# Kernel tuning notes

Hardware: AMD Instinct MI355X
Metric: run time of the kernel (lower is better)

Reference implementation:

```python
import jax, jax.numpy as jnp
from jax import lax
import numpy as np

BN_INV = 1.0 / np.sqrt(1.0 + 1e-5)  # eval-mode BatchNorm with running mean 0, var 1


def gather_points(x, idx):
    # x: [B, N, C]; idx: [B, ...] int -> [B, ..., C]
    bi = jnp.arange(x.shape[0]).reshape((x.shape[0],) + (1,) * (idx.ndim - 1))
    return x[bi, idx]


def fps(xyz, npoint):
    # furthest point sampling starting at index 0. xyz: [B, N, 3] -> [B, npoint] int32
    B, N, _ = xyz.shape

    def step(carry, _):
        dist, last = carry
        lx = jnp.take_along_axis(xyz, last[:, None, None], axis=1)  # [B,1,3]
        d = jnp.sum((xyz - lx) ** 2, axis=-1)                       # [B,N]
        dist = jnp.minimum(dist, d)
        nxt = jnp.argmax(dist, axis=-1).astype(jnp.int32)
        return (dist, nxt), nxt

    first = jnp.zeros((B,), jnp.int32)
    dist0 = jnp.full((B, N), 1e10, xyz.dtype)
    _, rest = lax.scan(step, (dist0, first), None, length=npoint - 1)
    return jnp.concatenate([first[None], rest], axis=0).T  # [B, npoint]


def ball_query(radius, nsample, xyz, new_xyz):
    # first nsample points (in index order) within radius of each query; pad with first hit
    N = xyz.shape[1]
    d2 = jnp.sum((new_xyz[:, :, None, :] - xyz[:, None, :, :]) ** 2, axis=-1)  # [B,S,N]
    mask = d2 < radius * radius
    key = jnp.where(mask, jnp.arange(N, dtype=jnp.int32), N)
    idx_sorted = jnp.sort(key, axis=-1)[..., :nsample]                          # [B,S,ns]
    cnt = jnp.sum(mask, axis=-1, keepdims=True)                                 # [B,S,1]
    idx = jnp.where(jnp.arange(nsample) < cnt, idx_sorted, idx_sorted[..., :1])
    return jnp.minimum(idx, N - 1)


def bn_relu(x, gamma, beta):
    # eval-mode BN (running mean 0 / var 1) + ReLU; channels on the last axis
    return jax.nn.relu(x * (gamma * BN_INV) + beta)


def sa_module(xyz, feats, npoint, radius, nsample, layers):
    # xyz [B,N,3], feats [B,C,N] -> (new_xyz [B,S,3], new_feats [B,Cout,S])
    fidx = fps(xyz, npoint)
    new_xyz = gather_points(xyz, fidx)                      # [B,S,3]
    gidx = ball_query(radius, nsample, xyz, new_xyz)        # [B,S,ns]
    g_xyz = gather_points(xyz, gidx) - new_xyz[:, :, None, :]   # [B,S,ns,3]
    g_feat = gather_points(jnp.swapaxes(feats, 1, 2), gidx)     # [B,S,ns,C]
    h = jnp.concatenate([g_xyz, g_feat], axis=-1)               # use_xyz=True
    for (w, g, b) in layers:                                    # shared MLP (1x1 conv2d+BN+ReLU)
        h = bn_relu(jnp.einsum('bsnc,oc->bsno', h, w), g, b)
    return new_xyz, jnp.swapaxes(jnp.max(h, axis=2), 1, 2)      # max-pool over nsample


def fp_module(unk_xyz, kn_xyz, unk_feats, kn_feats, layers):
    # three-NN weighted interpolation (squared distances, as the CUDA op) + unit conv MLP
    d2 = jnp.sum((unk_xyz[:, :, None, :] - kn_xyz[:, None, :, :]) ** 2, axis=-1)
    neg, idx = lax.top_k(-d2, 3)                 # 3 nearest known points
    w = 1.0 / (-neg + 1e-8)
    w = w / jnp.sum(w, axis=-1, keepdims=True)   # [B,Nu,3]
    kf = gather_points(jnp.swapaxes(kn_feats, 1, 2), idx)       # [B,Nu,3,C]
    interp = jnp.sum(kf * w[..., None], axis=2)                 # [B,Nu,C]
    h = jnp.concatenate([interp, jnp.swapaxes(unk_feats, 1, 2)], axis=-1)
    for (wt, g, b) in layers:
        h = bn_relu(jnp.einsum('bnc,oc->bno', h, wt), g, b)
    return jnp.swapaxes(h, 1, 2)                                # [B,Cout,Nu]


def setup_inputs() -> dict:
    key = jax.random.key(0)
    it = iter(jax.random.split(key, 80))
    B, N = 16, 4096
    d = {
        'xyz': jax.random.uniform(next(it), (B, N, 3), jnp.float32) * 0.3,
        'feats': jax.random.normal(next(it), (B, N, 3), jnp.float32),
    }
    specs = {'sa1': [(6, 64), (64, 128)], 'sa2': [(131, 128), (128, 256)],
             'sa3': [(259, 256), (256, 512)], 'fp3': [(768, 256), (256, 256)],
             'fp2': [(384, 128), (128, 128)], 'fp1': [(131, 128), (128, 128)]}
    for name, layers in specs.items():
        for i, (ci, co) in enumerate(layers):
            d[f'{name}_w{i}'] = jax.random.normal(next(it), (co, ci), jnp.float32) / np.sqrt(ci)
            d[f'{name}_g{i}'] = 1.0 + 0.1 * jax.random.normal(next(it), (co,), jnp.float32)
            d[f'{name}_b{i}'] = 0.1 * jax.random.normal(next(it), (co,), jnp.float32)
    d['fin_w'] = jax.random.normal(next(it), (512, 128), jnp.float32) / np.sqrt(128.0)
    d['fin_b'] = 0.1 * jax.random.normal(next(it), (512,), jnp.float32)
    d['fin_g'] = 1.0 + 0.1 * jax.random.normal(next(it), (512,), jnp.float32)
    d['fin_be'] = 0.1 * jax.random.normal(next(it), (512,), jnp.float32)
    return d


def reference(xyz, feats,
              sa1_w0, sa1_g0, sa1_b0, sa1_w1, sa1_g1, sa1_b1,
              sa2_w0, sa2_g0, sa2_b0, sa2_w1, sa2_g1, sa2_b1,
              sa3_w0, sa3_g0, sa3_b0, sa3_w1, sa3_g1, sa3_b1,
              fp3_w0, fp3_g0, fp3_b0, fp3_w1, fp3_g1, fp3_b1,
              fp2_w0, fp2_g0, fp2_b0, fp2_w1, fp2_g1, fp2_b1,
              fp1_w0, fp1_g0, fp1_b0, fp1_w1, fp1_g1, fp1_b1,
              fin_w, fin_b, fin_g, fin_be):
    f0 = jnp.swapaxes(feats, 1, 2)  # [B,3,N], channel-first like the torch module
    l1x, l1f = sa_module(xyz, f0, 256, 0.04, 16,
                         [(sa1_w0, sa1_g0, sa1_b0), (sa1_w1, sa1_g1, sa1_b1)])
    l2x, l2f = sa_module(l1x, l1f, 64, 0.08, 16,
                         [(sa2_w0, sa2_g0, sa2_b0), (sa2_w1, sa2_g1, sa2_b1)])
    l3x, l3f = sa_module(l2x, l2f, 16, 0.16, 16,
                         [(sa3_w0, sa3_g0, sa3_b0), (sa3_w1, sa3_g1, sa3_b1)])
    l2f = fp_module(l2x, l3x, l2f, l3f, [(fp3_w0, fp3_g0, fp3_b0), (fp3_w1, fp3_g1, fp3_b1)])
    l1f = fp_module(l1x, l2x, l1f, l2f, [(fp2_w0, fp2_g0, fp2_b0), (fp2_w1, fp2_g1, fp2_b1)])
    l0f = fp_module(xyz, l1x, f0, l1f, [(fp1_w0, fp1_g0, fp1_b0), (fp1_w1, fp1_g1, fp1_b1)])
    # final Conv1d(128->512, bias) + BN + ReLU
    h = jnp.einsum('bcn,oc->bon', l0f, fin_w) + fin_b[None, :, None]
    h = jax.nn.relu(h * (fin_g * BN_INV)[None, :, None] + fin_be[None, :, None])
    B, C, N = h.shape
    return jnp.swapaxes(h, 1, 2).reshape(B * N, C)  # un-batched per-point features
```

## Files before the change

### kernel.cpp

```cpp
#include <hip/hip_runtime.h>

#define DEVI __device__ __forceinline__
typedef unsigned long long u64;

static constexpr float BN_INV_F = 0.9999950000374997f;

DEVI float d2rn(float ax, float ay, float az, float bx, float by, float bz) {
    float dx = __fsub_rn(ax, bx), dy = __fsub_rn(ay, by), dz = __fsub_rn(az, bz);
    return __fadd_rn(__fadd_rn(__fmul_rn(dx, dx), __fmul_rn(dy, dy)), __fmul_rn(dz, dz));
}

DEVI u64 shfl_xor_u64(u64 x, int m) {
    unsigned lo = (unsigned)x, hi = (unsigned)(x >> 32);
    lo = (unsigned)__shfl_xor((int)lo, m, 64);
    hi = (unsigned)__shfl_xor((int)hi, m, 64);
    return ((u64)hi << 32) | lo;
}
DEVI u64 umin64(u64 a, u64 b) { return a < b ? a : b; }
DEVI u64 umax64(u64 a, u64 b) { return a > b ? a : b; }

template <int N, int NPOINT, int BS>
DEVI void fps_impl(const float* __restrict__ xyz, int* __restrict__ fidx) {
    constexpr int PPT = N / BS;
    constexpr int NW = BS / 64;
    __shared__ float4 xs4[N];
    __shared__ u64 wmax[2][NW > 1 ? NW : 1];
    const int t = threadIdx.x, b = blockIdx.x, lane = t & 63, wv = t >> 6;
    const float* xb = xyz + (size_t)b * N * 3;
    for (int p = t; p < N; p += BS)
        xs4[p] = make_float4(xb[p * 3], xb[p * 3 + 1], xb[p * 3 + 2], 0.f);
    if (t == 0) fidx[b * NPOINT] = 0;
    __syncthreads();
    float px[PPT], py[PPT], pz[PPT], dist[PPT];
#pragma unroll
    for (int i = 0; i < PPT; ++i) {
        float4 v = xs4[i * BS + t];
        px[i] = v.x; py[i] = v.y; pz[i] = v.z;
        dist[i] = 1e10f;
    }
    float4 q0 = xs4[0];
    float qx = q0.x, qy = q0.y, qz = q0.z;
    for (int it = 1; it < NPOINT; ++it) {
        float bestd = -1.f;
        unsigned bestidx = 0u;
#pragma unroll
        for (int i = 0; i < PPT; ++i) {
            float d = d2rn(px[i], py[i], pz[i], qx, qy, qz);
            float nd = fminf(dist[i], d);
            dist[i] = nd;
            if (nd > bestd) { bestd = nd; bestidx = (unsigned)(i * BS + t); }
        }
        u64 best = ((u64)__float_as_uint(bestd) << 32) | (0xFFFFFFFFu - bestidx);
#pragma unroll
        for (int m = 1; m < 64; m <<= 1) best = umax64(best, shfl_xor_u64(best, m));
        if constexpr (NW > 1) {
            if (lane == 0) wmax[it & 1][wv] = best;
            __syncthreads();
            u64 m2 = wmax[it & 1][lane & (NW - 1)];
#pragma unroll
            for (int m = 1; m < NW; m <<= 1) m2 = umax64(m2, shfl_xor_u64(m2, m));
            best = m2;
        }
        int p = (int)(0xFFFFFFFFu - (unsigned)best);
        float4 qv = xs4[p];
        qx = qv.x; qy = qv.y; qz = qv.z;
        if (t == 0) fidx[b * NPOINT + it] = p;
    }
}

__global__ __launch_bounds__(256) void fps1_kernel(const float* __restrict__ x, int* __restrict__ f) { fps_impl<4096, 256, 256>(x, f); }
__global__ __launch_bounds__(64)  void fps2_kernel(const float* __restrict__ x, int* __restrict__ f) { fps_impl<256, 64, 64>(x, f); }
__global__ __launch_bounds__(64)  void fps3_kernel(const float* __restrict__ x, int* __restrict__ f) { fps_impl<64, 16, 64>(x, f); }

template <int TR, int XSTR, int KMAIN, int CIM, int CIF, int MOFF, int CO, int MODE,
          bool SIDE, int SOFF, int OSTR>
DEVI void gemm_phase(float* __restrict__ Xs, float* __restrict__ Ws,
                     const float* __restrict__ W,
                     const float* __restrict__ sA, const float* __restrict__ sB,
                     const float* __restrict__ fbias,
                     float* __restrict__ gout, int r0,
                     unsigned* __restrict__ mp, const float* __restrict__ side, int t) {
    constexpr int RT = TR / 16;
    constexpr int NCOL = (CO / 16 < 8) ? (CO / 16) : 8;
    constexpr int ROWS = 16 * NCOL;
    constexpr int CC = CO / ROWS;
    constexpr int NCH = KMAIN / 8;
    constexpr int NQ = CC * NCH;
    constexpr int PRE = ROWS / 32;
    constexpr int XSTR4 = XSTR / 4;
    constexpr int AC = (MODE == 0) ? CC : 1;
    const int tx = t & 15, ty = t >> 4;
    const int swz = ty & 3;
    float acc[AC][RT][NCOL];
    if constexpr (MODE == 0) {
#pragma unroll
        for (int a = 0; a < AC; ++a)
#pragma unroll
            for (int r = 0; r < RT; ++r)
#pragma unroll
                for (int i = 0; i < NCOL; ++i) acc[a][r][i] = 0.f;
    }
    float pre[PRE];
#pragma unroll
    for (int i = 0; i < PRE; ++i) {
        int e = t + 256 * i, row = e >> 3, kk = e & 7;
        pre[i] = (kk < CIM) ? W[(size_t)row * CIF + MOFF + kk] : 0.f;
    }
#pragma unroll
    for (int i = 0; i < PRE; ++i) {
        int e = t + 256 * i;
        Ws[(e >> 3) * 12 + (e & 7)] = pre[i];
    }
#pragma unroll
    for (int cc = 0; cc < CC; ++cc) {
        if constexpr (MODE != 0) {
#pragma unroll
            for (int r = 0; r < RT; ++r)
#pragma unroll
                for (int i = 0; i < NCOL; ++i) acc[0][r][i] = 0.f;
        }
        for (int kc = 0; kc < NCH; ++kc) {
            const int qq = cc * NCH + kc, buf = kc & 1;
            __syncthreads();
            if (qq + 1 < NQ) {
                const int cn = (qq + 1) / NCH, kn = ((qq + 1) % NCH) * 8;
#pragma unroll
                for (int i = 0; i < PRE; ++i) {
                    int e = t + 256 * i, row = e >> 3, k = kn + (e & 7);
                    pre[i] = (k < CIM) ? W[(size_t)(cn * ROWS + row) * CIF + MOFF + k] : 0.f;
                }
            }
            const float* wsb = Ws + buf * (ROWS * 12);
#pragma unroll
            for (int k4i = 0; k4i < 2; ++k4i) {
                const int c4 = kc * 2 + k4i;
                float4 wv[NCOL];
#pragma unroll
                for (int i = 0; i < NCOL; ++i)
                    wv[i] = *(const float4*)&wsb[(tx + 16 * i) * 12 + k4i * 4];
                float4 xv[RT];
#pragma unroll
                for (int r = 0; r < RT; ++r)
                    xv[r] = *(const float4*)&Xs[((ty * RT + r) * XSTR4 + (c4 ^ swz)) * 4];
#pragma unroll
                for (int r = 0; r < RT; ++r)
#pragma unroll
                    for (int i = 0; i < NCOL; ++i) {
                        const int a = (MODE == 0) ? cc : 0;
                        acc[a][r][i] = fmaf(xv[r].x, wv[i].x, acc[a][r][i]);
                        acc[a][r][i] = fmaf(xv[r].y, wv[i].y, acc[a][r][i]);
                        acc[a][r][i] = fmaf(xv[r].z, wv[i].z, acc[a][r][i]);
                        acc[a][r][i] = fmaf(xv[r].w, wv[i].w, acc[a][r][i]);
                    }
            }
            if (qq + 1 < NQ) {
                float* wsn = Ws + (buf ^ 1) * (ROWS * 12);
#pragma unroll
                for (int i = 0; i < PRE; ++i) {
                    int e = t + 256 * i;
                    wsn[(e >> 3) * 12 + (e & 7)] = pre[i];
                }
            }
        }
        if constexpr (MODE == 1) {
#pragma unroll
            for (int i = 0; i < NCOL; ++i) {
                int c = cc * ROWS + tx + 16 * i;
                float bia = fbias ? fbias[c] : 0.f;
                float sc = sA[c] * BN_INV_F, be = sB[c];
#pragma unroll
                for (int r = 0; r < RT; ++r) {
                    float val = fmaxf(fmaf(acc[0][r][i] + bia, sc, be), 0.f);
                    gout[(size_t)(r0 + ty * RT + r) * OSTR + c] = val;
                }
            }
        } else if constexpr (MODE == 2) {
#pragma unroll
            for (int i = 0; i < NCOL; ++i) {
                int c = cc * ROWS + tx + 16 * i;
                float sc = sA[c] * BN_INV_F, bb = sB[c];
#pragma unroll
                for (int r = 0; r < RT; ++r) {
                    float val = fmaxf(fmaf(acc[0][r][i], sc, bb), 0.f);
                    atomicMax(&mp[((ty * RT + r) >> 4) * CO + c], __float_as_uint(val));
                }
            }
        }
    }
    if constexpr (MODE == 0) {
        if constexpr (SIDE) {
#pragma unroll
            for (int cc = 0; cc < AC; ++cc)
#pragma unroll
                for (int i = 0; i < NCOL; ++i) {
                    int c = cc * ROWS + tx + 16 * i;
#pragma unroll
                    for (int j = 0; j < 3; ++j) {
                        float wj = W[(size_t)c * CIF + SOFF + j];
#pragma unroll
                        for (int r = 0; r < RT; ++r)
                            acc[cc][r][i] = fmaf(side[(ty * RT + r) * 3 + j], wj,
                                                 acc[cc][r][i]);
                    }
                }
        }
        __syncthreads();
#pragma unroll
        for (int cc = 0; cc < AC; ++cc)
#pragma unroll
            for (int i = 0; i < NCOL; ++i) {
                int c = cc * ROWS + tx + 16 * i;
                float sc = sA[c] * BN_INV_F, bb = sB[c];
#pragma unroll
                for (int r = 0; r < RT; ++r) {
                    int row = ty * RT + r;
                    Xs[(row * XSTR4 + ((c >> 2) ^ swz)) * 4 + (c & 3)] =
                        fmaxf(fmaf(acc[cc][r][i], sc, bb), 0.f);
                }
            }
        __syncthreads();
    }
}

template <int N, int S, int CIN, int C1, int C2, int TR, bool USE_SIDE>
DEVI void sa_impl(const float* __restrict__ xyz, const float* __restrict__ feats,
                  const int* __restrict__ fidx,
                  const float* __restrict__ w0, const float* __restrict__ g0, const float* __restrict__ b0,
                  const float* __restrict__ w1, const float* __restrict__ g1, const float* __restrict__ b1,
                  float* __restrict__ oxyz, float* __restrict__ ofeat, float r2) {
    constexpr int QPB = TR / 16;
    constexpr int CIF = 3 + CIN;
    constexpr int KMAIN = USE_SIDE ? CIN : 16;
    constexpr int XSTR = (KMAIN > C1) ? KMAIN : C1;
    constexpr int XSTR4 = XSTR / 4;
    constexpr int RT = TR / 16;
    __shared__ __align__(16) float Xs[TR * XSTR];
    __shared__ __align__(16) float Ws[2 * 128 * 12];
    __shared__ int ids[QPB][16];
    __shared__ float qp[QPB][3];
    __shared__ unsigned mp[QPB * C2];
    __shared__ float side[USE_SIDE ? TR * 3 : 4];
    const int t = threadIdx.x, lane = t & 63, wv = t >> 6;
    const int q0 = blockIdx.x * QPB;
    for (int q = wv; q < QPB; q += 4) {
        const int sq = q0 + q, bb = sq / S;
        const float* xb = xyz + (size_t)bb * N * 3;
        const int qi = fidx[sq];
        const float qx = xb[qi * 3], qy = xb[qi * 3 + 1], qz = xb[qi * 3 + 2];
        if (lane == 0) {
            qp[q][0] = qx; qp[q][1] = qy; qp[q][2] = qz;
            float* op = oxyz + (size_t)sq * 3;
            op[0] = qx; op[1] = qy; op[2] = qz;
        }
        int base = 0;
        for (int seg = 0; seg < N; seg += 64) {
            const int p = seg + lane;
            float d = d2rn(xb[p * 3], xb[p * 3 + 1], xb[p * 3 + 2], qx, qy, qz);
            bool hit = d < r2;
            u64 mask = __ballot(hit);
            int before = (int)__popcll(mask & ((1ull << lane) - 1ull));
            if (hit && base + before < 16) ids[q][base + before] = p;
            base += (int)__popcll(mask);
            if (base >= 16) break;
        }
        if (lane == 0) {
            int cnt = base < 16 ? base : 16;
            int first = ids[q][0];
            for (int r = cnt; r < 16; ++r) ids[q][r] = first;
        }
    }
    __syncthreads();
    if constexpr (!USE_SIDE) {
        for (int e = t; e < TR * 16; e += 256) {
            int j = e >> 4, c = e & 15;
            int q = j >> 4, p = ids[q][j & 15];
            int bb = (q0 + q) / S;
            float v = 0.f;
            if (c < 3) v = __fsub_rn(xyz[((size_t)bb * N + p) * 3 + c], qp[q][c]);
            else if (c < 6) v = feats[((size_t)bb * N + p) * CIN + (c - 3)];
            Xs[(j * XSTR4 + ((c >> 2) ^ ((j / RT) & 3))) * 4 + (c & 3)] = v;
        }
    } else {
        constexpr int C4N = CIN / 4;
        for (int e = t; e < TR * C4N; e += 256) {
            int j = e / C4N, c4 = e % C4N;
            int q = j >> 4, p = ids[q][j & 15];
            int bb = (q0 + q) / S;
            float4 v = *(const float4*)&feats[((size_t)bb * N + p) * CIN + c4 * 4];
            *(float4*)&Xs[(j * XSTR4 + (c4 ^ ((j / RT) & 3))) * 4] = v;
        }
        for (int e = t; e < TR * 3; e += 256) {
            int j = e / 3, c = e % 3;
            int q = j >> 4, p = ids[q][j & 15];
            int bb = (q0 + q) / S;
            side[e] = __fsub_rn(xyz[((size_t)bb * N + p) * 3 + c], qp[q][c]);
        }
    }
    for (int e = t; e < QPB * C2; e += 256) mp[e] = 0u;
    gemm_phase<TR, XSTR, KMAIN, (USE_SIDE ? CIN : 6), CIF, (USE_SIDE ? 3 : 0),
               C1, 0, USE_SIDE, 0, 0>(Xs, Ws, w0, g0, b0, nullptr, nullptr, 0,
                                      nullptr, side, t);
    gemm_phase<TR, XSTR, C1, C1, C1, 0, C2, 2, false, 0, 0>(
        Xs, Ws, w1, g1, b1, nullptr, nullptr, 0, mp, nullptr, t);
    __syncthreads();
    for (int e = t; e < QPB * C2; e += 256)
        ofeat[(size_t)q0 * C2 + e] = __uint_as_float(mp[e]);
}

#define SA_ARGS const float* __restrict__ xyz, const float* __restrict__ feats, \
                const int* __restrict__ fidx, \
                const float* __restrict__ w0, const float* __restrict__ g0, const float* __restrict__ b0, \
                const float* __restrict__ w1, const float* __restrict__ g1, const float* __restrict__ b1, \
                float* __restrict__ oxyz, float* __restrict__ ofeat, float r2
__global__ __launch_bounds__(256) void sa1_kernel(SA_ARGS) {
    sa_impl<4096, 256, 3, 64, 128, 64, false>(xyz, feats, fidx, w0, g0, b0, w1, g1, b1, oxyz, ofeat, r2);
}
__global__ __launch_bounds__(256) void sa2_kernel(SA_ARGS) {
    sa_impl<256, 64, 128, 128, 256, 64, true>(xyz, feats, fidx, w0, g0, b0, w1, g1, b1, oxyz, ofeat, r2);
}
__global__ __launch_bounds__(256) void sa3_kernel(SA_ARGS) {
    sa_impl<64, 16, 256, 256, 512, 16, true>(xyz, feats, fidx, w0, g0, b0, w1, g1, b1, oxyz, ofeat, r2);
}

template <int M, int CK, int CU, int C1, int C2, int TR>
DEVI void fp_impl(const float* __restrict__ uxyz, const float* __restrict__ kxyz,
                  const float* __restrict__ ufeat, const float* __restrict__ kfeat,
                  const float* __restrict__ w0, const float* __restrict__ g0, const float* __restrict__ b0,
                  const float* __restrict__ w1, const float* __restrict__ g1, const float* __restrict__ b1,
                  float* __restrict__ out, int NU) {
    constexpr int CH = CK + CU;
    constexpr int XSTR = CH;
    constexpr int XSTR4 = XSTR / 4;
    constexpr int RT = TR / 16;
    __shared__ __align__(16) float Xs[TR * XSTR];
    __shared__ __align__(16) float Ws[2 * 128 * 12];
    __shared__ float kxs[M * 3];
    const int t = threadIdx.x, lane = t & 63, wv = t >> 6;
    const int r0 = blockIdx.x * TR;
    const int b = r0 / NU;
    for (int e = t; e < M * 3; e += 256) kxs[e] = kxyz[(size_t)b * M * 3 + e];
    __syncthreads();
    for (int j = wv; j < TR; j += 4) {
        const int r = r0 + j;
        const int sw = (j / RT) & 3;
        const float* up = uxyz + (size_t)r * 3;
        float ux = up[0], uy = up[1], uz = up[2];
        u64 a0 = ~0ull, a1 = ~0ull, a2 = ~0ull;
        for (int k = lane; k < M; k += 64) {
            float d = d2rn(kxs[k * 3], kxs[k * 3 + 1], kxs[k * 3 + 2], ux, uy, uz);
            u64 key = ((u64)__float_as_uint(d) << 32) | (unsigned)k;
            if (key < a0)      { a2 = a1; a1 = a0; a0 = key; }
            else if (key < a1) { a2 = a1; a1 = key; }
            else if (key < a2) { a2 = key; }
        }
#pragma unroll
        for (int m = 1; m < 64; m <<= 1) {
            u64 b0k = shfl_xor_u64(a0, m), b1k = shfl_xor_u64(a1, m), b2k = shfl_xor_u64(a2, m);
            u64 c0 = umin64(a0, b0k);
            u64 c1 = umin64(umax64(a0, b0k), umin64(a1, b1k));
            u64 c2 = umin64(umin64(umax64(a1, b0k), umax64(a0, b1k)), umin64(a2, b2k));
            a0 = c0; a1 = c1; a2 = c2;
        }
        int s0 = (int)(unsigned)a0, s1 = (int)(unsigned)a1, s2 = (int)(unsigned)a2;
        float d0 = __uint_as_float((unsigned)(a0 >> 32));
        float d1 = __uint_as_float((unsigned)(a1 >> 32));
        float dd2 = __uint_as_float((unsigned)(a2 >> 32));
        float wa = 1.0f / (d0 + 1e-8f), wb = 1.0f / (d1 + 1e-8f), wc = 1.0f / (dd2 + 1e-8f);
        float sum = (wa + wb) + wc;
        wa /= sum; wb /= sum; wc /= sum;
        const float* kb = kfeat + (size_t)b * M * CK;
        for (int c4 = lane; c4 < CK / 4; c4 += 64) {
            float4 va = *(const float4*)(kb + (size_t)s0 * CK + c4 * 4);
            float4 vb = *(const float4*)(kb + (size_t)s1 * CK + c4 * 4);
            float4 vc = *(const float4*)(kb + (size_t)s2 * CK + c4 * 4);
            float4 rr;
            rr.x = va.x * wa + vb.x * wb + vc.x * wc;
            rr.y = va.y * wa + vb.y * wb + vc.y * wc;
            rr.z = va.z * wa + vb.z * wb + vc.z * wc;
            rr.w = va.w * wa + vb.w * wb + vc.w * wc;
            *(float4*)&Xs[(j * XSTR4 + (c4 ^ sw)) * 4] = rr;
        }
        for (int c4 = CK / 4 + lane; c4 < CH / 4; c4 += 64) {
            float4 v = *(const float4*)&ufeat[(size_t)r * CU + (c4 * 4 - CK)];
            *(float4*)&Xs[(j * XSTR4 + (c4 ^ sw)) * 4] = v;
        }
    }
    gemm_phase<TR, XSTR, CH, CH, CH, 0, C1, 0, false, 0, 0>(
        Xs, Ws, w0, g0, b0, nullptr, nullptr, 0, nullptr, nullptr, t);
    gemm_phase<TR, XSTR, C1, C1, C1, 0, C2, 1, false, 0, C2>(
        Xs, Ws, w1, g1, b1, nullptr, out, r0, nullptr, nullptr, t);
}

#define FP_ARGS const float* __restrict__ uxyz, const float* __restrict__ kxyz, \
                const float* __restrict__ ufeat, const float* __restrict__ kfeat, \
                const float* __restrict__ w0, const float* __restrict__ g0, const float* __restrict__ b0, \
                const float* __restrict__ w1, const float* __restrict__ g1, const float* __restrict__ b1, \
                float* __restrict__ out, int NU
__global__ __launch_bounds__(256) void fp3_kernel(FP_ARGS) {
    fp_impl<16, 512, 256, 256, 256, 16>(uxyz, kxyz, ufeat, kfeat, w0, g0, b0, w1, g1, b1, out, NU);
}
__global__ __launch_bounds__(256) void fp2_kernel(FP_ARGS) {
    fp_impl<64, 256, 128, 128, 128, 16>(uxyz, kxyz, ufeat, kfeat, w0, g0, b0, w1, g1, b1, out, NU);
}

__global__ __launch_bounds__(256) void fp1_mlp_kernel(
    const float* __restrict__ uxyz, const float* __restrict__ kxyz,
    const float* __restrict__ ufeat3, const float* __restrict__ kfeat,
    const float* __restrict__ w0, const float* __restrict__ g0, const float* __restrict__ b0,
    const float* __restrict__ w1, const float* __restrict__ g1, const float* __restrict__ b1,
    float* __restrict__ out) {
    constexpr int TR = 128, M = 256, CK = 128;
    __shared__ __align__(16) float Xs[TR * 128];
    __shared__ __align__(16) float Ws[2 * 128 * 12];
    __shared__ float side[TR * 3];
    __shared__ float wgt2[TR * 2];
    __shared__ unsigned pidx[TR];
    const int t = threadIdx.x;
    const int r0 = blockIdx.x * TR;
    const int b = r0 >> 12;
    for (int e = t; e < TR * 3; e += 256) side[e] = ufeat3[(size_t)r0 * 3 + e];
    const int g = t >> 2, sub = t & 3;
    const float* kb3 = kxyz + (size_t)b * M * 3;
    for (int row = g; row < TR; row += 64) {
        const float* up = uxyz + (size_t)(r0 + row) * 3;
        float ux = up[0], uy = up[1], uz = up[2];
        u64 a0 = ~0ull, a1 = ~0ull, a2 = ~0ull;
        for (int k = sub; k < M; k += 4) {
            float d = d2rn(kb3[k * 3], kb3[k * 3 + 1], kb3[k * 3 + 2], ux, uy, uz);
            u64 key = ((u64)__float_as_uint(d) << 32) | (unsigned)k;
            if (key < a0)      { a2 = a1; a1 = a0; a0 = key; }
            else if (key < a1) { a2 = a1; a1 = key; }
            else if (key < a2) { a2 = key; }
        }
#pragma unroll
        for (int m = 1; m < 4; m <<= 1) {
            u64 b0k = shfl_xor_u64(a0, m), b1k = shfl_xor_u64(a1, m), b2k = shfl_xor_u64(a2, m);
            u64 c0 = umin64(a0, b0k);
            u64 c1 = umin64(umax64(a0, b0k), umin64(a1, b1k));
            u64 c2 = umin64(umin64(umax64(a1, b0k), umax64(a0, b1k)), umin64(a2, b2k));
            a0 = c0; a1 = c1; a2 = c2;
        }
        if (sub == 0) {
            unsigned s0 = (unsigned)a0 & 255u, s1 = (unsigned)a1 & 255u, s2 = (unsigned)a2 & 255u;
            float d0 = __uint_as_float((unsigned)(a0 >> 32));
            float d1 = __uint_as_float((unsigned)(a1 >> 32));
            float dd2 = __uint_as_float((unsigned)(a2 >> 32));
            float wa = 1.0f / (d0 + 1e-8f), wb = 1.0f / (d1 + 1e-8f), wc = 1.0f / (dd2 + 1e-8f);
            float sum = (wa + wb) + wc;
            wa /= sum; wb /= sum;
            pidx[row] = s0 | (s1 << 8) | (s2 << 16);
            wgt2[row * 2] = wa; wgt2[row * 2 + 1] = wb;
        }
    }
    __syncthreads();
    const float* kfb = kfeat + (size_t)b * M * CK;
    for (int e = t; e < TR * 32; e += 256) {
        int j = e >> 5, c4 = e & 31;
        unsigned u = pidx[j];
        int s0 = u & 255, s1 = (u >> 8) & 255, s2 = (u >> 16) & 255;
        float wa = wgt2[j * 2], wb = wgt2[j * 2 + 1], wc = 1.0f - wa - wb;
        float4 va = *(const float4*)(kfb + (size_t)s0 * CK + c4 * 4);
        float4 vb = *(const float4*)(kfb + (size_t)s1 * CK + c4 * 4);
        float4 vc = *(const float4*)(kfb + (size_t)s2 * CK + c4 * 4);
        float4 rr;
        rr.x = va.x * wa + vb.x * wb + vc.x * wc;
        rr.y = va.y * wa + vb.y * wb + vc.y * wc;
        rr.z = va.z * wa + vb.z * wb + vc.z * wc;
        rr.w = va.w * wa + vb.w * wb + vc.w * wc;
        *(float4*)&Xs[(j * 32 + (c4 ^ ((j >> 3) & 3))) * 4] = rr;
    }
    gemm_phase<TR, 128, 128, 128, 131, 0, 128, 0, true, 128, 0>(
        Xs, Ws, w0, g0, b0, nullptr, nullptr, 0, nullptr, side, t);
    gemm_phase<TR, 128, 128, 128, 128, 0, 128, 1, false, 0, 512>(
        Xs, Ws, w1, g1, b1, nullptr, out, r0, nullptr, nullptr, t);
}

__global__ __launch_bounds__(256) void fin_kernel(
    float* io,
    const float* __restrict__ fw, const float* __restrict__ fb,
    const float* __restrict__ fg, const float* __restrict__ fbe) {
    __shared__ __align__(16) float Xs[128 * 128];
    __shared__ __align__(16) float Ws[2 * 128 * 12];
    const int t = threadIdx.x, tx = t & 15, ty = t >> 4;
    const int r0 = blockIdx.x * 128;
    const int swz = ty & 3;
    for (int e = t; e < 128 * 32; e += 256) {
        int j = e >> 5, c4 = e & 31;
        float4 v = *(const float4*)&io[(size_t)(r0 + j) * 512 + c4 * 4];
        *(float4*)&Xs[(j * 32 + (c4 ^ ((j >> 3) & 3))) * 4] = v;
    }
    for (int nt = 0; nt < 4; ++nt) {
        const int c0 = nt * 128;
        float acc[8][8];
#pragma unroll
        for (int r = 0; r < 8; ++r)
#pragma unroll
            for (int i = 0; i < 8; ++i) acc[r][i] = 0.f;
        float wpre[4];
#pragma unroll
        for (int i = 0; i < 4; ++i) {
            int e = t + 256 * i, row = e >> 3, kk = e & 7;
            wpre[i] = fw[(size_t)(c0 + row) * 128 + kk];
        }
#pragma unroll
        for (int i = 0; i < 4; ++i) {
            int e = t + 256 * i;
            Ws[(e >> 3) * 12 + (e & 7)] = wpre[i];
        }
        for (int kc = 0; kc < 16; ++kc) {
            const int buf = kc & 1;
            __syncthreads();
            if (kc < 15) {
                const int kn = (kc + 1) * 8;
#pragma unroll
                for (int i = 0; i < 4; ++i) {
                    int e = t + 256 * i, row = e >> 3, kk = e & 7;
                    wpre[i] = fw[(size_t)(c0 + row) * 128 + kn + kk];
                }
            }
            const float* wsb = Ws + buf * 1536;
#pragma unroll
            for (int k4i = 0; k4i < 2; ++k4i) {
                const int c4 = kc * 2 + k4i;
                float4 wv[8];
#pragma unroll
                for (int i = 0; i < 8; ++i)
                    wv[i] = *(const float4*)&wsb[(tx + 16 * i) * 12 + k4i * 4];
                float4 xv[8];
#pragma unroll
                for (int r = 0; r < 8; ++r)
                    xv[r] = *(const float4*)&Xs[((ty * 8 + r) * 32 + (c4 ^ swz)) * 4];
#pragma unroll
                for (int r = 0; r < 8; ++r)
#pragma unroll
                    for (int i = 0; i < 8; ++i) {
                        acc[r][i] = fmaf(xv[r].x, wv[i].x, acc[r][i]);
                        acc[r][i] = fmaf(xv[r].y, wv[i].y, acc[r][i]);
                        acc[r][i] = fmaf(xv[r].z, wv[i].z, acc[r][i]);
                        acc[r][i] = fmaf(xv[r].w, wv[i].w, acc[r][i]);
                    }
            }
            if (kc < 15) {
                float* wsn = Ws + (buf ^ 1) * 1536;
#pragma unroll
                for (int i = 0; i < 4; ++i) {
                    int e = t + 256 * i;
                    wsn[(e >> 3) * 12 + (e & 7)] = wpre[i];
                }
            }
        }
#pragma unroll
        for (int i = 0; i < 8; ++i) {
            int c = c0 + tx + 16 * i;
            float bia = fb[c], sc = fg[c] * BN_INV_F, be = fbe[c];
#pragma unroll
            for (int r = 0; r < 8; ++r) {
                float val = fmaxf(fmaf(acc[r][i] + bia, sc, be), 0.f);
                io[(size_t)(r0 + ty * 8 + r) * 512 + c] = val;
            }
        }
    }
}

extern "C" void kernel_launch(void* const* d_in, const int* in_sizes, int n_in,
                              void* d_out, int out_size, void* d_ws, size_t ws_size,
                              hipStream_t stream) {
    (void)in_sizes; (void)n_in; (void)out_size; (void)ws_size;
    const float* xyz   = (const float*)d_in[0];
    const float* feats = (const float*)d_in[1];
    const float* sa1_w0 = (const float*)d_in[2];
    const float* sa1_g0 = (const float*)d_in[3];
    const float* sa1_b0 = (const float*)d_in[4];
    const float* sa1_w1 = (const float*)d_in[5];
    const float* sa1_g1 = (const float*)d_in[6];
    const float* sa1_b1 = (const float*)d_in[7];
    const float* sa2_w0 = (const float*)d_in[8];
    const float* sa2_g0 = (const float*)d_in[9];
    const float* sa2_b0 = (const float*)d_in[10];
    const float* sa2_w1 = (const float*)d_in[11];
    const float* sa2_g1 = (const float*)d_in[12];
    const float* sa2_b1 = (const float*)d_in[13];
    const float* sa3_w0 = (const float*)d_in[14];
    const float* sa3_g0 = (const float*)d_in[15];
    const float* sa3_b0 = (const float*)d_in[16];
    const float* sa3_w1 = (const float*)d_in[17];
    const float* sa3_g1 = (const float*)d_in[18];
    const float* sa3_b1 = (const float*)d_in[19];
    const float* fp3_w0 = (const float*)d_in[20];
    const float* fp3_g0 = (const float*)d_in[21];
    const float* fp3_b0 = (const float*)d_in[22];
    const float* fp3_w1 = (const float*)d_in[23];
    const float* fp3_g1 = (const float*)d_in[24];
    const float* fp3_b1 = (const float*)d_in[25];
    const float* fp2_w0 = (const float*)d_in[26];
    const float* fp2_g0 = (const float*)d_in[27];
    const float* fp2_b0 = (const float*)d_in[28];
    const float* fp2_w1 = (const float*)d_in[29];
    const float* fp2_g1 = (const float*)d_in[30];
    const float* fp2_b1 = (const float*)d_in[31];
    const float* fp1_w0 = (const float*)d_in[32];
    const float* fp1_g0 = (const float*)d_in[33];
    const float* fp1_b0 = (const float*)d_in[34];
    const float* fp1_w1 = (const float*)d_in[35];
    const float* fp1_g1 = (const float*)d_in[36];
    const float* fp1_b1 = (const float*)d_in[37];
    const float* fin_w  = (const float*)d_in[38];
    const float* fin_b  = (const float*)d_in[39];
    const float* fin_g  = (const float*)d_in[40];
    const float* fin_be = (const float*)d_in[41];

    float* ws = (float*)d_ws;
    float* l1x  = ws;
    float* l1f  = l1x + 12288;
    float* l2x  = l1f + 524288;
    float* l2f  = l2x + 3072;
    float* l3x  = l2f + 262144;
    float* l3f  = l3x + 768;
    float* l2fb = l3f + 131072;
    float* l1fb = l2fb + 262144;
    int* fidx1 = (int*)(l1fb + 524288);
    int* fidx2 = fidx1 + 4096;
    int* fidx3 = fidx2 + 1024;

    const float R2_1 = (float)(0.04 * 0.04);
    const float R2_2 = (float)(0.08 * 0.08);
    const float R2_3 = (float)(0.16 * 0.16);

    fps1_kernel<<<16, 256, 0, stream>>>(xyz, fidx1);
    sa1_kernel<<<1024, 256, 0, stream>>>(
        xyz, feats, fidx1, sa1_w0, sa1_g0, sa1_b0, sa1_w1, sa1_g1, sa1_b1,
        l1x, l1f, R2_1);

    fps2_kernel<<<16, 64, 0, stream>>>(l1x, fidx2);
    sa2_kernel<<<256, 256, 0, stream>>>(
        l1x, l1f, fidx2, sa2_w0, sa2_g0, sa2_b0, sa2_w1, sa2_g1, sa2_b1,
        l2x, l2f, R2_2);

    fps3_kernel<<<16, 64, 0, stream>>>(l2x, fidx3);
    sa3_kernel<<<256, 256, 0, stream>>>(
        l2x, l2f, fidx3, sa3_w0, sa3_g0, sa3_b0, sa3_w1, sa3_g1, sa3_b1,
        l3x, l3f, R2_3);

    fp3_kernel<<<64, 256, 0, stream>>>(
        l2x, l3x, l2f, l3f, fp3_w0, fp3_g0, fp3_b0, fp3_w1, fp3_g1, fp3_b1,
        l2fb, 64);

    fp2_kernel<<<256, 256, 0, stream>>>(
        l1x, l2x, l1f, l2fb, fp2_w0, fp2_g0, fp2_b0, fp2_w1, fp2_g1, fp2_b1,
        l1fb, 256);

    fp1_mlp_kernel<<<512, 256, 0, stream>>>(
        xyz, l1x, feats, l1fb, fp1_w0, fp1_g0, fp1_b0, fp1_w1, fp1_g1, fp1_b1,
        (float*)d_out);

    fin_kernel<<<512, 256, 0, stream>>>(
        (float*)d_out, fin_w, fin_b, fin_g, fin_be);
}
```

Measured before the change: 805.0 us.

## Fuse all three FPS stages into one kernel keeping sampled points in LDS

Replaces the three separate furthest-point-sampling kernels with one kernel per batch. After the level-1 FPS it runs the level-2 and level-3 FPS on a single wavefront, using the selected points held in shared memory, and writes l1x/l2x/l3x directly. The SA kernels no longer write the sampled coordinates. This removes two kernel launches and their serialized dependency on the SA kernels, at the cost of three wavefronts idling while the small FPS stages run.

```diff
diff --git a/kernel.cpp b/kernel.cpp
--- a/kernel.cpp
+++ b/kernel.cpp
@@ -19,17 +19,20 @@
 DEVI u64 umin64(u64 a, u64 b) { return a < b ? a : b; }
 DEVI u64 umax64(u64 a, u64 b) { return a > b ? a : b; }
 
-template <int N, int NPOINT, int BS>
-DEVI void fps_impl(const float* __restrict__ xyz, int* __restrict__ fidx) {
-    constexpr int PPT = N / BS;
-    constexpr int NW = BS / 64;
+__global__ __launch_bounds__(256) void fps_all_kernel(
+    const float* __restrict__ xyz, int* __restrict__ fidx1,
+    int* __restrict__ fidx2, int* __restrict__ fidx3,
+    float* __restrict__ l1x, float* __restrict__ l2x, float* __restrict__ l3x) {
+    constexpr int N = 4096, NP1 = 256, BS = 256, PPT = 16, NW = 4;
     __shared__ float4 xs4[N];
-    __shared__ u64 wmax[2][NW > 1 ? NW : 1];
+    __shared__ float4 sel1[NP1];
+    __shared__ float4 sel2[64];
+    __shared__ u64 wmax[2][NW];
     const int t = threadIdx.x, b = blockIdx.x, lane = t & 63, wv = t >> 6;
     const float* xb = xyz + (size_t)b * N * 3;
     for (int p = t; p < N; p += BS)
         xs4[p] = make_float4(xb[p * 3], xb[p * 3 + 1], xb[p * 3 + 2], 0.f);
-    if (t == 0) fidx[b * NPOINT] = 0;
+    if (t == 0) fidx1[b * NP1] = 0;
     __syncthreads();
     float px[PPT], py[PPT], pz[PPT], dist[PPT];
 #pragma unroll
@@ -40,7 +43,12 @@
     }
     float4 q0 = xs4[0];
     float qx = q0.x, qy = q0.y, qz = q0.z;
-    for (int it = 1; it < NPOINT; ++it) {
+    if (t == 0) {
+        sel1[0] = q0;
+        float* o = l1x + (size_t)b * NP1 * 3;
+        o[0] = q0.x; o[1] = q0.y; o[2] = q0.z;
+    }
+    for (int it = 1; it < NP1; ++it) {
         float bestd = -1.f;
         unsigned bestidx = 0u;
 #pragma unroll
@@ -53,24 +61,91 @@
         u64 best = ((u64)__float_as_uint(bestd) << 32) | (0xFFFFFFFFu - bestidx);
 #pragma unroll
         for (int m = 1; m < 64; m <<= 1) best = umax64(best, shfl_xor_u64(best, m));
-        if constexpr (NW > 1) {
-            if (lane == 0) wmax[it & 1][wv] = best;
-            __syncthreads();
-            u64 m2 = wmax[it & 1][lane & (NW - 1)];
-#pragma unroll
-            for (int m = 1; m < NW; m <<= 1) m2 = umax64(m2, shfl_xor_u64(m2, m));
-            best = m2;
-        }
+        if (lane == 0) wmax[it & 1][wv] = best;
+        __syncthreads();
+        u64 m2 = wmax[it & 1][lane & (NW - 1)];
+#pragma unroll
+        for (int m = 1; m < NW; m <<= 1) m2 = umax64(m2, shfl_xor_u64(m2, m));
+        best = m2;
         int p = (int)(0xFFFFFFFFu - (unsigned)best);
         float4 qv = xs4[p];
         qx = qv.x; qy = qv.y; qz = qv.z;
-        if (t == 0) fidx[b * NPOINT + it] = p;
-    }
-}
-
-__global__ __launch_bounds__(256) void fps1_kernel(const float* __restrict__ x, int* __restrict__ f) { fps_impl<4096, 256, 256>(x, f); }
-__global__ __launch_bounds__(64)  void fps2_kernel(const float* __restrict__ x, int* __restrict__ f) { fps_impl<256, 64, 64>(x, f); }
-__global__ __launch_bounds__(64)  void fps3_kernel(const float* __restrict__ x, int* __restrict__ f) { fps_impl<64, 16, 64>(x, f); }
+        if (t == 0) {
+            fidx1[b * NP1 + it] = p;
+            sel1[it] = qv;
+            float* o = l1x + ((size_t)b * NP1 + it) * 3;
+            o[0] = qv.x; o[1] = qv.y; o[2] = qv.z;
+        }
+    }
+    if (wv != 0) return;
+    {
+        float p2x[4], p2y[4], p2z[4], d2v[4];
+#pragma unroll
+        for (int i = 0; i < 4; ++i) {
+            float4 v = sel1[i * 64 + lane];
+            p2x[i] = v.x; p2y[i] = v.y; p2z[i] = v.z;
+            d2v[i] = 1e10f;
+        }
+        float4 q = sel1[0];
+        float ax = q.x, ay = q.y, az = q.z;
+        if (lane == 0) {
+            fidx2[b * 64] = 0;
+            sel2[0] = q;
+            float* o = l2x + (size_t)b * 64 * 3;
+            o[0] = q.x; o[1] = q.y; o[2] = q.z;
+        }
+        for (int it = 1; it < 64; ++it) {
+            float bestd = -1.f;
+            unsigned bestidx = 0u;
+#pragma unroll
+            for (int i = 0; i < 4; ++i) {
+                float d = d2rn(p2x[i], p2y[i], p2z[i], ax, ay, az);
+                float nd = fminf(d2v[i], d);
+                d2v[i] = nd;
+                if (nd > bestd) { bestd = nd; bestidx = (unsigned)(i * 64 + lane); }
+            }
+            u64 best = ((u64)__float_as_uint(bestd) << 32) | (0xFFFFFFFFu - bestidx);
+#pragma unroll
+            for (int m = 1; m < 64; m <<= 1) best = umax64(best, shfl_xor_u64(best, m));
+            int p = (int)(0xFFFFFFFFu - (unsigned)best);
+            float4 qv = sel1[p];
+            ax = qv.x; ay = qv.y; az = qv.z;
+            if (lane == 0) {
+                fidx2[b * 64 + it] = p;
+                sel2[it] = qv;
+                float* o = l2x + ((size_t)b * 64 + it) * 3;
+                o[0] = qv.x; o[1] = qv.y; o[2] = qv.z;
+            }
+        }
+    }
+    {
+        float4 v = sel2[lane];
+        float p3x = v.x, p3y = v.y, p3z = v.z, d3 = 1e10f;
+        float4 q = sel2[0];
+        float ax = q.x, ay = q.y, az = q.z;
+        if (lane == 0) {
+            fidx3[b * 16] = 0;
+            float* o = l3x + (size_t)b * 16 * 3;
+            o[0] = q.x; o[1] = q.y; o[2] = q.z;
+        }
+        for (int it = 1; it < 16; ++it) {
+            float d = d2rn(p3x, p3y, p3z, ax, ay, az);
+            float nd = fminf(d3, d);
+            d3 = nd;
+            u64 best = ((u64)__float_as_uint(nd) << 32) | (0xFFFFFFFFu - (unsigned)lane);
+#pragma unroll
+            for (int m = 1; m < 64; m <<= 1) best = umax64(best, shfl_xor_u64(best, m));
+            int p = (int)(0xFFFFFFFFu - (unsigned)best);
+            float4 qv = sel2[p];
+            ax = qv.x; ay = qv.y; az = qv.z;
+            if (lane == 0) {
+                fidx3[b * 16 + it] = p;
+                float* o = l3x + ((size_t)b * 16 + it) * 3;
+                o[0] = qv.x; o[1] = qv.y; o[2] = qv.z;
+            }
+        }
+    }
+}
 
 template <int TR, int XSTR, int KMAIN, int CIM, int CIF, int MOFF, int CO, int MODE,
           bool SIDE, int SOFF, int OSTR>
@@ -227,7 +302,7 @@
                   const int* __restrict__ fidx,
                   const float* __restrict__ w0, const float* __restrict__ g0, const float* __restrict__ b0,
                   const float* __restrict__ w1, const float* __restrict__ g1, const float* __restrict__ b1,
-                  float* __restrict__ oxyz, float* __restrict__ ofeat, float r2) {
+                  float* __restrict__ ofeat, float r2) {
     constexpr int QPB = TR / 16;
     constexpr int CIF = 3 + CIN;
     constexpr int KMAIN = USE_SIDE ? CIN : 16;
@@ -249,8 +324,6 @@
         const float qx = xb[qi * 3], qy = xb[qi * 3 + 1], qz = xb[qi * 3 + 2];
         if (lane == 0) {
             qp[q][0] = qx; qp[q][1] = qy; qp[q][2] = qz;
-            float* op = oxyz + (size_t)sq * 3;
-            op[0] = qx; op[1] = qy; op[2] = qz;
         }
         int base = 0;
         for (int seg = 0; seg < N; seg += 64) {
@@ -311,15 +384,15 @@
                 const int* __restrict__ fidx, \
                 const float* __restrict__ w0, const float* __restrict__ g0, const float* __restrict__ b0, \
                 const float* __restrict__ w1, const float* __restrict__ g1, const float* __restrict__ b1, \
-                float* __restrict__ oxyz, float* __restrict__ ofeat, float r2
+                float* __restrict__ ofeat, float r2
 __global__ __launch_bounds__(256) void sa1_kernel(SA_ARGS) {
-    sa_impl<4096, 256, 3, 64, 128, 64, false>(xyz, feats, fidx, w0, g0, b0, w1, g1, b1, oxyz, ofeat, r2);
+    sa_impl<4096, 256, 3, 64, 128, 64, false>(xyz, feats, fidx, w0, g0, b0, w1, g1, b1, ofeat, r2);
 }
 __global__ __launch_bounds__(256) void sa2_kernel(SA_ARGS) {
-    sa_impl<256, 64, 128, 128, 256, 64, true>(xyz, feats, fidx, w0, g0, b0, w1, g1, b1, oxyz, ofeat, r2);
+    sa_impl<256, 64, 128, 128, 256, 64, true>(xyz, feats, fidx, w0, g0, b0, w1, g1, b1, ofeat, r2);
 }
 __global__ __launch_bounds__(256) void sa3_kernel(SA_ARGS) {
-    sa_impl<64, 16, 256, 256, 512, 16, true>(xyz, feats, fidx, w0, g0, b0, w1, g1, b1, oxyz, ofeat, r2);
+    sa_impl<64, 16, 256, 256, 512, 16, true>(xyz, feats, fidx, w0, g0, b0, w1, g1, b1, ofeat, r2);
 }
 
 template <int M, int CK, int CU, int C1, int C2, int TR>
@@ -626,20 +699,17 @@
     const float R2_2 = (float)(0.08 * 0.08);
     const float R2_3 = (float)(0.16 * 0.16);
 
-    fps1_kernel<<<16, 256, 0, stream>>>(xyz, fidx1);
+    fps_all_kernel<<<16, 256, 0, stream>>>(xyz, fidx1, fidx2, fidx3, l1x, l2x, l3x);
+
     sa1_kernel<<<1024, 256, 0, stream>>>(
         xyz, feats, fidx1, sa1_w0, sa1_g0, sa1_b0, sa1_w1, sa1_g1, sa1_b1,
-        l1x, l1f, R2_1);
-
-    fps2_kernel<<<16, 64, 0, stream>>>(l1x, fidx2);
+        l1f, R2_1);
     sa2_kernel<<<256, 256, 0, stream>>>(
         l1x, l1f, fidx2, sa2_w0, sa2_g0, sa2_b0, sa2_w1, sa2_g1, sa2_b1,
-        l2x, l2f, R2_2);
-
-    fps3_kernel<<<16, 64, 0, stream>>>(l2x, fidx3);
+        l2f, R2_2);
     sa3_kernel<<<256, 256, 0, stream>>>(
         l2x, l2f, fidx3, sa3_w0, sa3_g0, sa3_b0, sa3_w1, sa3_g1, sa3_b1,
-        l3x, l3f, R2_3);
+        l3f, R2_3);
 
     fp3_kernel<<<64, 256, 0, stream>>>(
         l2x, l3x, l2f, l3f, fp3_w0, fp3_g0, fp3_b0, fp3_w1, fp3_g1, fp3_b1,
```

Result: no change. 807.6 us (+0.3%).
